# Optimization experiments

Hardware: AMD Instinct MI355X
Metric: run time of the kernel (lower is better)

## Reference

```python
import jax, jax.numpy as jnp
import numpy as np

B, M, K = 32, 64, 36
DS, DX, DQ, H = 512, 128, 512, 256


def setup_inputs() -> dict:
    key = jax.random.key(0)
    ks = jax.random.split(key, 11)
    sc = lambda fan_in: 1.0 / np.sqrt(fan_in)
    return {
        "s2": jax.random.normal(ks[0], (B, M, DS), jnp.float32),
        "x0": jax.random.normal(ks[1], (B, K, DX), jnp.float32),
        "q": jax.random.normal(ks[2], (B, DQ), jnp.float32),
        # score MLP: Linear(DS+DX+DQ -> H), ReLU, Linear(H -> 1)
        "score_w1": jax.random.normal(ks[3], (DS + DX + DQ, H), jnp.float32) * sc(DS + DX + DQ),
        "score_b1": jax.random.normal(ks[4], (H,), jnp.float32) * 0.01,
        "score_w2": jax.random.normal(ks[5], (H, 1), jnp.float32) * sc(H),
        "score_b2": jax.random.normal(ks[6], (1,), jnp.float32) * 0.01,
        # h MLP: Linear(DS -> H), ReLU, Linear(H -> DX)
        "h_w1": jax.random.normal(ks[7], (DS, H), jnp.float32) * sc(DS),
        "h_b1": jax.random.normal(ks[8], (H,), jnp.float32) * 0.01,
        "h_w2": jax.random.normal(ks[9], (H, DX), jnp.float32) * sc(H),
        "h_b2": jax.random.normal(ks[10], (DX,), jnp.float32) * 0.01,
    }


def reference(s2, x0, q, score_w1, score_b1, score_w2, score_b2, h_w1, h_b1, h_w2, h_b2):
    ds = s2.shape[-1]
    dx = x0.shape[-1]
    # First score Linear over concat [s_exp, x_exp, q_exp] decomposes into
    # block matmuls (same math as Linear on the concat, no 4D concat tensor).
    w_s = score_w1[:ds]            # (DS, H)
    w_x = score_w1[ds:ds + dx]     # (DX, H)
    w_q = score_w1[ds + dx:]       # (DQ, H)
    pre_s = jnp.einsum('bmd,dh->bmh', s2, w_s)   # (b, m, H)
    pre_x = jnp.einsum('bkd,dh->bkh', x0, w_x)   # (b, k, H)
    pre_q = q @ w_q                              # (b, H)
    hidden = jax.nn.relu(pre_s[:, :, None, :] + pre_x[:, None, :, :]
                         + pre_q[:, None, None, :] + score_b1)  # (b, m, k, H)
    logits = jnp.einsum('bmkh,h->bmk', hidden, score_w2[:, 0]) + score_b2[0]
    att = jax.nn.softmax(logits, axis=1)         # softmax over m
    h_s = jax.nn.relu(s2 @ h_w1 + h_b1) @ h_w2 + h_b2  # (b, m, DX)
    agg = jnp.einsum('bmk,bmf->bkf', att, h_s)   # (b, k, DX)
    return jnp.concatenate([x0, agg], axis=-1)   # (b, k, 2*DX)
```

## Files before the change

### kernel.cpp

```cpp
#include <hip/hip_runtime.h>

#define B_  32
#define M_  64
#define K_  36
#define DS_ 512
#define DX_ 128
#define DQ_ 512
#define H_  256

#define S2B 1024
#define PXB 288
#define QPB 32

__global__ __launch_bounds__(512, 6) void kern1(
    const float* __restrict__ s2,
    const float* __restrict__ x0,
    const float* __restrict__ q,
    const float* __restrict__ score_w1,
    const float* __restrict__ score_b1,
    const float* __restrict__ h_w1,
    const float* __restrict__ h_b1,
    float* __restrict__ pre_s,
    float* __restrict__ h1r,
    float* __restrict__ px,
    float* __restrict__ qpre)
{
    __shared__ float comb[4 * H_];
    const int t   = threadIdx.x;
    const int bid = blockIdx.x;
    const int h   = t & 255;
    const int kh  = __builtin_amdgcn_readfirstlane(t >> 8);

    if (bid < S2B) {
        const int tile = bid >> 1, mat = bid & 1;
        const float* W  = mat ? h_w1 : score_w1;
        const float* A  = s2 + (size_t)tile * 4 * DS_ + kh * 256;
        const float* Wp = W + (size_t)(kh * 256) * H_ + h;

        float acc[4];
        #pragma unroll
        for (int r = 0; r < 4; ++r) acc[r] = 0.f;

        #pragma unroll 2
        for (int k = 0; k < 256; k += 4) {
            const float b0 = Wp[(size_t)(k + 0) * H_];
            const float b1 = Wp[(size_t)(k + 1) * H_];
            const float b2 = Wp[(size_t)(k + 2) * H_];
            const float b3 = Wp[(size_t)(k + 3) * H_];
            #pragma unroll
            for (int r = 0; r < 4; ++r) {
                const float4 a = *(const float4*)(A + (size_t)r * DS_ + k);
                acc[r] = fmaf(a.x, b0, acc[r]);
                acc[r] = fmaf(a.y, b1, acc[r]);
                acc[r] = fmaf(a.z, b2, acc[r]);
                acc[r] = fmaf(a.w, b3, acc[r]);
            }
        }
        if (kh) {
            #pragma unroll
            for (int r = 0; r < 4; ++r) comb[r * H_ + h] = acc[r];
        }
        __syncthreads();
        if (!kh) {
            if (!mat) {
                float* dst = pre_s + (size_t)tile * 4 * H_ + h;
                #pragma unroll
                for (int r = 0; r < 4; ++r)
                    dst[(size_t)r * H_] = acc[r] + comb[r * H_ + h];
            } else {
                const float b1v = h_b1[h];
                float* dst = h1r + (size_t)tile * 4 * H_ + h;
                #pragma unroll
                for (int r = 0; r < 4; ++r)
                    dst[(size_t)r * H_] =
                        fmaxf(acc[r] + comb[r * H_ + h] + b1v, 0.f);
            }
        }

    } else if (bid < S2B + PXB) {
        const int tile = bid - S2B;
        const float* A  = x0 + (size_t)tile * 4 * DX_ + kh * 64;
        const float* Wp = score_w1 + (size_t)(DS_ + kh * 64) * H_ + h;

        float acc[4];
        #pragma unroll
        for (int r = 0; r < 4; ++r) acc[r] = 0.f;

        #pragma unroll 2
        for (int k = 0; k < 64; k += 4) {
            const float b0 = Wp[(size_t)(k + 0) * H_];
            const float b1 = Wp[(size_t)(k + 1) * H_];
            const float b2 = Wp[(size_t)(k + 2) * H_];
            const float b3 = Wp[(size_t)(k + 3) * H_];
            #pragma unroll
            for (int r = 0; r < 4; ++r) {
                const float4 a = *(const float4*)(A + (size_t)r * DX_ + k);
                acc[r] = fmaf(a.x, b0, acc[r]);
                acc[r] = fmaf(a.y, b1, acc[r]);
                acc[r] = fmaf(a.z, b2, acc[r]);
                acc[r] = fmaf(a.w, b3, acc[r]);
            }
        }
        if (kh) {
            #pragma unroll
            for (int r = 0; r < 4; ++r) comb[r * H_ + h] = acc[r];
        }
        __syncthreads();
        if (!kh) {
            const float b1v = score_b1[h];
            float* dst = px + (size_t)tile * 4 * H_ + h;
            #pragma unroll
            for (int r = 0; r < 4; ++r)
                dst[(size_t)r * H_] = acc[r] + comb[r * H_ + h] + b1v;
        }

    } else {
        const int b = bid - (S2B + PXB);
        const float* qp = q + (size_t)b * DQ_ + kh * 256;
        const float* wq = score_w1 + (size_t)(DS_ + DX_ + kh * 256) * H_ + h;
        float a0 = 0.f, a1 = 0.f, a2 = 0.f, a3 = 0.f;
        #pragma unroll 2
        for (int d = 0; d < 256; d += 4) {
            const float4 q4 = *(const float4*)(qp + d);
            a0 = fmaf(q4.x, wq[(size_t)(d + 0) * H_], a0);
            a1 = fmaf(q4.y, wq[(size_t)(d + 1) * H_], a1);
            a2 = fmaf(q4.z, wq[(size_t)(d + 2) * H_], a2);
            a3 = fmaf(q4.w, wq[(size_t)(d + 3) * H_], a3);
        }
        const float s = (a0 + a1) + (a2 + a3);
        if (kh) comb[h] = s;
        __syncthreads();
        if (!kh) qpre[(size_t)b * H_ + h] = s + comb[h];
    }
}

__global__ __launch_bounds__(256) void kern2(
    const float* __restrict__ h1r,
    const float* __restrict__ h_w2,
    float* __restrict__ hs)
{
    __shared__ float A[4 * H_];
    __shared__ float part[4][DX_];
    const int t  = threadIdx.x;
    const int r0 = blockIdx.x * 4;

    {
        const int flat = t * 4;
        *(float4*)&A[flat] = *(const float4*)(h1r + (size_t)r0 * H_ + flat);
    }
    __syncthreads();

    const int fq  = (t & 31) * 4;
    const int g   = t >> 5;
    const int row = g & 3, kh = g >> 2;
    const float* ap = &A[row * H_ + kh * 128];
    const float* wp = h_w2 + (size_t)(kh * 128) * DX_ + fq;

    float4 acc = {0.f, 0.f, 0.f, 0.f};
    #pragma unroll 4
    for (int d = 0; d < 128; d += 4) {
        const float a0 = ap[d], a1 = ap[d + 1], a2 = ap[d + 2], a3 = ap[d + 3];
        const float4 w0  = *(const float4*)(wp + (size_t)(d + 0) * DX_);
        const float4 w1  = *(const float4*)(wp + (size_t)(d + 1) * DX_);
        const float4 w2v = *(const float4*)(wp + (size_t)(d + 2) * DX_);
        const float4 w3  = *(const float4*)(wp + (size_t)(d + 3) * DX_);
        acc.x = fmaf(a0, w0.x, acc.x); acc.y = fmaf(a0, w0.y, acc.y);
        acc.z = fmaf(a0, w0.z, acc.z); acc.w = fmaf(a0, w0.w, acc.w);
        acc.x = fmaf(a1, w1.x, acc.x); acc.y = fmaf(a1, w1.y, acc.y);
        acc.z = fmaf(a1, w1.z, acc.z); acc.w = fmaf(a1, w1.w, acc.w);
        acc.x = fmaf(a2, w2v.x, acc.x); acc.y = fmaf(a2, w2v.y, acc.y);
        acc.z = fmaf(a2, w2v.z, acc.z); acc.w = fmaf(a2, w2v.w, acc.w);
        acc.x = fmaf(a3, w3.x, acc.x); acc.y = fmaf(a3, w3.y, acc.y);
        acc.z = fmaf(a3, w3.z, acc.z); acc.w = fmaf(a3, w3.w, acc.w);
    }
    if (kh) *(float4*)&part[row][fq] = acc;
    __syncthreads();
    if (!kh) {
        const float4 p = *(const float4*)&part[row][fq];
        float4 o;
        o.x = acc.x + p.x; o.y = acc.y + p.y;
        o.z = acc.z + p.z; o.w = acc.w + p.w;
        *(float4*)(hs + (size_t)(r0 + row) * DX_ + fq) = o;
    }
}

__global__ __launch_bounds__(256) void kern3(
    const float* __restrict__ pre_s,
    const float* __restrict__ px,
    const float* __restrict__ qpre,
    const float* __restrict__ score_w2,
    const float* __restrict__ hs,
    const float* __restrict__ h_b2,
    const float* __restrict__ x0,
    float* __restrict__ out)
{
    __shared__ float logit[M_];
    __shared__ float att[M_];
    __shared__ float pr[DX_];

    const int t    = threadIdx.x;
    const int bk   = blockIdx.x;
    const int b    = bk / K_;
    const int lane = t & 63, wave = t >> 6;
    const int hq   = lane << 2;
    const int f    = t & 127, mh = t >> 7;

    float4 c4, v4;
    {
        const float4 qv = *(const float4*)(qpre + (size_t)b * H_ + hq);
        const float4 pv = *(const float4*)(px + (size_t)bk * H_ + hq);
        c4.x = qv.x + pv.x; c4.y = qv.y + pv.y;
        c4.z = qv.z + pv.z; c4.w = qv.w + pv.w;
        v4 = *(const float4*)(score_w2 + hq);
    }

    float hv[32];
    {
        const float* hsp = hs + ((size_t)b * M_ + mh * 32) * DX_ + f;
        #pragma unroll
        for (int m2 = 0; m2 < 32; ++m2)
            hv[m2] = hsp[(size_t)m2 * DX_];
    }

    const float* ps = pre_s + (size_t)b * M_ * H_;
    #pragma unroll 2
    for (int mi = 0; mi < 16; ++mi) {
        const int m = wave * 16 + mi;
        const float4 p = *(const float4*)(ps + (size_t)m * H_ + hq);
        float x = fmaxf(p.x + c4.x, 0.f) * v4.x
                + fmaxf(p.y + c4.y, 0.f) * v4.y
                + fmaxf(p.z + c4.z, 0.f) * v4.z
                + fmaxf(p.w + c4.w, 0.f) * v4.w;
        #pragma unroll
        for (int off = 32; off > 0; off >>= 1)
            x += __shfl_xor(x, off, 64);
        if (lane == 0) logit[m] = x;
    }
    __syncthreads();

    if (wave == 0) {
        const float L = logit[lane];
        float mx = L;
        #pragma unroll
        for (int off = 32; off > 0; off >>= 1)
            mx = fmaxf(mx, __shfl_xor(mx, off, 64));
        const float e = expf(L - mx);
        float sm = e;
        #pragma unroll
        for (int off = 32; off > 0; off >>= 1)
            sm += __shfl_xor(sm, off, 64);
        att[lane] = e / sm;
    }
    __syncthreads();

    {
        float r = 0.f;
        #pragma unroll
        for (int m2 = 0; m2 < 32; ++m2)
            r = fmaf(att[mh * 32 + m2], hv[m2], r);
        if (mh) pr[f] = r;
        __syncthreads();
        if (!mh)
            out[(size_t)bk * (2 * DX_) + DX_ + f] = r + pr[f] + h_b2[f];
    }
    if (t < DX_)
        out[(size_t)bk * (2 * DX_) + t] = x0[(size_t)bk * DX_ + t];
}

extern "C" void kernel_launch(void* const* d_in, const int* in_sizes, int n_in,
                              void* d_out, int out_size, void* d_ws, size_t ws_size,
                              hipStream_t stream) {
    (void)in_sizes; (void)n_in; (void)out_size; (void)ws_size;
    const float* s2       = (const float*)d_in[0];
    const float* x0       = (const float*)d_in[1];
    const float* q        = (const float*)d_in[2];
    const float* score_w1 = (const float*)d_in[3];
    const float* score_b1 = (const float*)d_in[4];
    const float* score_w2 = (const float*)d_in[5];
    const float* h_w1     = (const float*)d_in[7];
    const float* h_b1     = (const float*)d_in[8];
    const float* h_w2     = (const float*)d_in[9];
    const float* h_b2     = (const float*)d_in[10];
    float* out = (float*)d_out;

    float* ws    = (float*)d_ws;
    float* pre_s = ws;
    float* h1r   = pre_s + (size_t)B_ * M_ * H_;
    float* px    = h1r   + (size_t)B_ * M_ * H_;
    float* qpre  = px    + (size_t)B_ * K_ * H_;
    float* hs    = qpre  + (size_t)B_ * H_;

    kern1<<<S2B + PXB + QPB, 512, 0, stream>>>(
        s2, x0, q, score_w1, score_b1, h_w1, h_b1, pre_s, h1r, px, qpre);
    kern2<<<512, 256, 0, stream>>>(h1r, h_w2, hs);
    kern3<<<B_ * K_, 256, 0, stream>>>(pre_s, px, qpre, score_w2, hs, h_b2,
                                       x0, out);
}
```

Measured before the change: 127.2 us.

## Move s2 projections onto bf16x3 MFMA with a pre-pack kernel

After: 119.4 us (median of 2 runs). 6.1% less time.

```diff
diff --git a/kernel.cpp b/kernel.cpp
--- a/kernel.cpp
+++ b/kernel.cpp
@@ -8,77 +8,81 @@
 #define DQ_ 512
 #define H_  256
 
-#define S2B 1024
-#define PXB 288
-#define QPB 32
-
-__global__ __launch_bounds__(512, 6) void kern1(
+typedef __attribute__((ext_vector_type(8))) short short8v;
+typedef __attribute__((ext_vector_type(4))) float float4v;
+
+#define PK_S2 128
+#define PK_W  32
+#define PXB   288
+#define QPB   32
+
+__global__ __launch_bounds__(512) void kernP(
     const float* __restrict__ s2,
     const float* __restrict__ x0,
     const float* __restrict__ q,
     const float* __restrict__ score_w1,
     const float* __restrict__ score_b1,
     const float* __restrict__ h_w1,
-    const float* __restrict__ h_b1,
-    float* __restrict__ pre_s,
-    float* __restrict__ h1r,
+    unsigned short* __restrict__ Apk_h,
+    unsigned short* __restrict__ Apk_l,
+    unsigned short* __restrict__ Bpk_h,
+    unsigned short* __restrict__ Bpk_l,
     float* __restrict__ px,
     float* __restrict__ qpre)
 {
     __shared__ float comb[4 * H_];
     const int t   = threadIdx.x;
     const int bid = blockIdx.x;
-    const int h   = t & 255;
-    const int kh  = __builtin_amdgcn_readfirstlane(t >> 8);
-
-    if (bid < S2B) {
-        const int tile = bid >> 1, mat = bid & 1;
-        const float* W  = mat ? h_w1 : score_w1;
-        const float* A  = s2 + (size_t)tile * 4 * DS_ + kh * 256;
-        const float* Wp = W + (size_t)(kh * 256) * H_ + h;
-
-        float acc[4];
-        #pragma unroll
-        for (int r = 0; r < 4; ++r) acc[r] = 0.f;
-
-        #pragma unroll 2
-        for (int k = 0; k < 256; k += 4) {
-            const float b0 = Wp[(size_t)(k + 0) * H_];
-            const float b1 = Wp[(size_t)(k + 1) * H_];
-            const float b2 = Wp[(size_t)(k + 2) * H_];
-            const float b3 = Wp[(size_t)(k + 3) * H_];
-            #pragma unroll
-            for (int r = 0; r < 4; ++r) {
-                const float4 a = *(const float4*)(A + (size_t)r * DS_ + k);
-                acc[r] = fmaf(a.x, b0, acc[r]);
-                acc[r] = fmaf(a.y, b1, acc[r]);
-                acc[r] = fmaf(a.z, b2, acc[r]);
-                acc[r] = fmaf(a.w, b3, acc[r]);
-            }
-        }
-        if (kh) {
-            #pragma unroll
-            for (int r = 0; r < 4; ++r) comb[r * H_ + h] = acc[r];
-        }
-        __syncthreads();
-        if (!kh) {
-            if (!mat) {
-                float* dst = pre_s + (size_t)tile * 4 * H_ + h;
-                #pragma unroll
-                for (int r = 0; r < 4; ++r)
-                    dst[(size_t)r * H_] = acc[r] + comb[r * H_ + h];
-            } else {
-                const float b1v = h_b1[h];
-                float* dst = h1r + (size_t)tile * 4 * H_ + h;
-                #pragma unroll
-                for (int r = 0; r < 4; ++r)
-                    dst[(size_t)r * H_] =
-                        fmaxf(acc[r] + comb[r * H_ + h] + b1v, 0.f);
-            }
-        }
-
-    } else if (bid < S2B + PXB) {
-        const int tile = bid - S2B;
+
+    if (bid < PK_S2) {
+        const int rt = bid;
+        const float* src = s2 + (size_t)rt * 16 * DS_;
+        unsigned short* dh = Apk_h + (size_t)rt * 8192;
+        unsigned short* dl = Apk_l + (size_t)rt * 8192;
+        #pragma unroll 4
+        for (int j = 0; j < 16; ++j) {
+            const int f  = t * 16 + j;
+            const int i  = f & 7;
+            const int l  = (f >> 3) & 63;
+            const int ks = f >> 9;
+            const int row = l & 15;
+            const int k  = ks * 32 + ((l >> 4) << 2) + (i & 3) + ((i >> 2) << 4);
+            const float a = src[(size_t)row * DS_ + k];
+            const unsigned u  = __float_as_uint(a);
+            const unsigned short hi = (unsigned short)(u >> 16);
+            const float res = a - __uint_as_float((unsigned)hi << 16);
+            const unsigned short lo =
+                (unsigned short)(__float_as_uint(res) >> 16);
+            dh[f] = hi; dl[f] = lo;
+        }
+
+    } else if (bid < PK_S2 + PK_W) {
+        const int wi  = bid - PK_S2;
+        const int mat = wi >> 4, nt = wi & 15;
+        const float* Wsrc = mat ? h_w1 : score_w1;
+        unsigned short* dh = Bpk_h + (size_t)wi * 8192;
+        unsigned short* dl = Bpk_l + (size_t)wi * 8192;
+        #pragma unroll 4
+        for (int j = 0; j < 16; ++j) {
+            const int f  = t * 16 + j;
+            const int i  = f & 7;
+            const int l  = (f >> 3) & 63;
+            const int ks = f >> 9;
+            const int col = nt * 16 + (l & 15);
+            const int k  = ks * 32 + ((l >> 4) << 2) + (i & 3) + ((i >> 2) << 4);
+            const float a = Wsrc[(size_t)k * H_ + col];
+            const unsigned u  = __float_as_uint(a);
+            const unsigned short hi = (unsigned short)(u >> 16);
+            const float res = a - __uint_as_float((unsigned)hi << 16);
+            const unsigned short lo =
+                (unsigned short)(__float_as_uint(res) >> 16);
+            dh[f] = hi; dl[f] = lo;
+        }
+
+    } else if (bid < PK_S2 + PK_W + PXB) {
+        const int tile = bid - (PK_S2 + PK_W);
+        const int h    = t & 255;
+        const int kh   = __builtin_amdgcn_readfirstlane(t >> 8);
         const float* A  = x0 + (size_t)tile * 4 * DX_ + kh * 64;
         const float* Wp = score_w1 + (size_t)(DS_ + kh * 64) * H_ + h;
 
@@ -115,7 +119,9 @@
         }
 
     } else {
-        const int b = bid - (S2B + PXB);
+        const int b  = bid - (PK_S2 + PK_W + PXB);
+        const int h  = t & 255;
+        const int kh = __builtin_amdgcn_readfirstlane(t >> 8);
         const float* qp = q + (size_t)b * DQ_ + kh * 256;
         const float* wq = score_w1 + (size_t)(DS_ + DX_ + kh * 256) * H_ + h;
         float a0 = 0.f, a1 = 0.f, a2 = 0.f, a3 = 0.f;
@@ -131,6 +137,71 @@
         if (kh) comb[h] = s;
         __syncthreads();
         if (!kh) qpre[(size_t)b * H_ + h] = s + comb[h];
+    }
+}
+
+__global__ __launch_bounds__(64) void kernG(
+    const unsigned short* __restrict__ Apk_h,
+    const unsigned short* __restrict__ Apk_l,
+    const unsigned short* __restrict__ Bpk_h,
+    const unsigned short* __restrict__ Bpk_l,
+    const float* __restrict__ h_b1,
+    float* __restrict__ pre_s,
+    float* __restrict__ h1r)
+{
+    const int l   = threadIdx.x;
+    const int bid = blockIdx.x;
+    const int ns  = bid & 7;
+    const int mat = (bid >> 3) & 1;
+    const int rt  = bid >> 4;
+
+    const short8v* Ah = (const short8v*)Apk_h + (size_t)rt * 16 * 64 + l;
+    const short8v* Al = (const short8v*)Apk_l + (size_t)rt * 16 * 64 + l;
+    const int nt0 = mat * 16 + ns * 2;
+    const short8v* B0h = (const short8v*)Bpk_h + (size_t)nt0 * 16 * 64 + l;
+    const short8v* B0l = (const short8v*)Bpk_l + (size_t)nt0 * 16 * 64 + l;
+    const short8v* B1h = B0h + 16 * 64;
+    const short8v* B1l = B0l + 16 * 64;
+
+    float4v aA0 = {0.f, 0.f, 0.f, 0.f}, aB0 = aA0, aC0 = aA0;
+    float4v aA1 = aA0, aB1 = aA0, aC1 = aA0;
+
+    #pragma unroll 2
+    for (int ks = 0; ks < 16; ++ks) {
+        const short8v ah  = Ah[(size_t)ks * 64];
+        const short8v al  = Al[(size_t)ks * 64];
+        const short8v b0h = B0h[(size_t)ks * 64];
+        const short8v b0l = B0l[(size_t)ks * 64];
+        const short8v b1h = B1h[(size_t)ks * 64];
+        const short8v b1l = B1l[(size_t)ks * 64];
+        aA0 = __builtin_amdgcn_mfma_f32_16x16x32_bf16(ah, b0h, aA0, 0, 0, 0);
+        aB0 = __builtin_amdgcn_mfma_f32_16x16x32_bf16(ah, b0l, aB0, 0, 0, 0);
+        aC0 = __builtin_amdgcn_mfma_f32_16x16x32_bf16(al, b0h, aC0, 0, 0, 0);
+        aA1 = __builtin_amdgcn_mfma_f32_16x16x32_bf16(ah, b1h, aA1, 0, 0, 0);
+        aB1 = __builtin_amdgcn_mfma_f32_16x16x32_bf16(ah, b1l, aB1, 0, 0, 0);
+        aC1 = __builtin_amdgcn_mfma_f32_16x16x32_bf16(al, b1h, aC1, 0, 0, 0);
+    }
+
+    const float4v s0 = aA0 + aB0 + aC0;
+    const float4v s1 = aA1 + aB1 + aC1;
+
+    const int row0 = rt * 16 + ((l >> 4) << 2);
+    const int c0   = ns * 32 + (l & 15);
+
+    if (!mat) {
+        #pragma unroll
+        for (int r = 0; r < 4; ++r) {
+            pre_s[(size_t)(row0 + r) * H_ + c0]      = s0[r];
+            pre_s[(size_t)(row0 + r) * H_ + c0 + 16] = s1[r];
+        }
+    } else {
+        const float bv0 = h_b1[c0];
+        const float bv1 = h_b1[c0 + 16];
+        #pragma unroll
+        for (int r = 0; r < 4; ++r) {
+            h1r[(size_t)(row0 + r) * H_ + c0]      = fmaxf(s0[r] + bv0, 0.f);
+            h1r[(size_t)(row0 + r) * H_ + c0 + 16] = fmaxf(s1[r] + bv1, 0.f);
+        }
     }
 }
 
@@ -290,8 +361,16 @@
     float* qpre  = px    + (size_t)B_ * K_ * H_;
     float* hs    = qpre  + (size_t)B_ * H_;
 
-    kern1<<<S2B + PXB + QPB, 512, 0, stream>>>(
-        s2, x0, q, score_w1, score_b1, h_w1, h_b1, pre_s, h1r, px, qpre);
+    unsigned short* Apk_h = (unsigned short*)(ws + 2097152);
+    unsigned short* Apk_l = Apk_h + (size_t)128 * 16 * 64 * 8;
+    unsigned short* Bpk_h = Apk_l + (size_t)128 * 16 * 64 * 8;
+    unsigned short* Bpk_l = Bpk_h + (size_t)32 * 16 * 64 * 8;
+
+    kernP<<<PK_S2 + PK_W + PXB + QPB, 512, 0, stream>>>(
+        s2, x0, q, score_w1, score_b1, h_w1,
+        Apk_h, Apk_l, Bpk_h, Bpk_l, px, qpre);
+    kernG<<<2048, 64, 0, stream>>>(Apk_h, Apk_l, Bpk_h, Bpk_l, h_b1,
+                                   pre_s, h1r);
     kern2<<<512, 256, 0, stream>>>(h1r, h_w2, hs);
     kern3<<<B_ * K_, 256, 0, stream>>>(pre_s, px, qpre, score_w2, hs, h_b2,
                                        x0, out);
```
